# Performance work log

Measured on AMD Instinct MI355X. Metric: run time of the kernel, lower is better.

Reference implementation:

```python
import jax, jax.numpy as jnp
import numpy as np

B, N, E, D, NS, H = 32, 4096, 256, 256, 8, 256
N_ITERS, N_SH, N_MESH, MESH_LR = 3, 5, 4, 5.0

def layer_norm(x, scale, bias, eps=1e-5):
    m = jnp.mean(x, axis=-1, keepdims=True)
    v = jnp.var(x, axis=-1, keepdims=True)
    return (x - m) / jnp.sqrt(v + eps) * scale + bias

def sinkhorn(C, a, b, u=None, v=None, n_iters=N_SH):
    # log-domain Sinkhorn with marginals a [B,N], b [B,S]; C [B,N,S]
    log_a, log_b = jnp.log(a), jnp.log(b)
    if u is None:
        u = jnp.zeros_like(a)
    if v is None:
        v = jnp.zeros_like(b)
    K = -C
    for _ in range(n_iters):
        u = log_a - jax.nn.logsumexp(K + v[:, None, :], axis=-1)
        v = log_b - jax.nn.logsumexp(K + u[:, :, None], axis=-2)
    attn = jnp.exp(K + u[:, :, None] + v[:, None, :])
    return attn, u, v

def minimize_entropy_of_sinkhorn(C0, a, b, mesh_lr=MESH_LR, n_mesh=N_MESH):
    # MESH: gradient-descend the cost matrix to minimize entropy of the transport plan
    def ent(C):
        attn, _, _ = sinkhorn(C, a, b)
        return -jnp.sum(attn * jnp.log(attn + 1e-8))
    C = C0
    for _ in range(n_mesh):
        C = C - mesh_lr * jax.grad(ent)(C)
    _, u, v = sinkhorn(C, a, b)
    return C, u, v

def gru_cell(x, h, Wih, Whh, bih, bhh):
    # torch.nn.GRUCell math, gate order (r, z, n)
    gi = x @ Wih.T + bih
    gh = h @ Whh.T + bhh
    ir, iz, inn = jnp.split(gi, 3, axis=-1)
    hr, hz, hn = jnp.split(gh, 3, axis=-1)
    r = jax.nn.sigmoid(ir + hr)
    z = jax.nn.sigmoid(iz + hz)
    n = jnp.tanh(inn + r * hn)
    return (1.0 - z) * n + z * h

def setup_inputs():
    key = jax.random.key(0)
    ks = jax.random.split(key, 16)
    s = 0.02
    return {
        "inputs": jax.random.normal(ks[0], (B, N, E), jnp.float32),
        "slots_init": jax.random.normal(ks[1], (B, NS, D), jnp.float32),
        "ln_in_s": jnp.ones((E,), jnp.float32), "ln_in_b": jnp.zeros((E,), jnp.float32),
        "ln_sl_s": jnp.ones((D,), jnp.float32), "ln_sl_b": jnp.zeros((D,), jnp.float32),
        "ln_mlp_s": jnp.ones((D,), jnp.float32), "ln_mlp_b": jnp.zeros((D,), jnp.float32),
        "Wq": jax.random.normal(ks[2], (D, D), jnp.float32) * s,
        "Wk": jax.random.normal(ks[3], (E, D), jnp.float32) * s,
        "Wv": jax.random.normal(ks[4], (E, D), jnp.float32) * s,
        "wi_W": jax.random.normal(ks[5], (E, 1), jnp.float32) * s, "wi_b": jnp.zeros((1,), jnp.float32),
        "ws_W": jax.random.normal(ks[6], (D, 1), jnp.float32) * s, "ws_b": jnp.zeros((1,), jnp.float32),
        "gru_Wih": jax.random.normal(ks[7], (3 * D, D), jnp.float32) * s,
        "gru_Whh": jax.random.normal(ks[8], (3 * D, D), jnp.float32) * s,
        "gru_bih": jnp.zeros((3 * D,), jnp.float32), "gru_bhh": jnp.zeros((3 * D,), jnp.float32),
        "mlp_W1": jax.random.normal(ks[9], (D, H), jnp.float32) * s, "mlp_b1": jnp.zeros((H,), jnp.float32),
        "mlp_W2": jax.random.normal(ks[10], (H, D), jnp.float32) * s, "mlp_b2": jnp.zeros((D,), jnp.float32),
    }

def reference(inputs, slots_init, ln_in_s, ln_in_b, ln_sl_s, ln_sl_b, ln_mlp_s, ln_mlp_b, Wq, Wk, Wv, wi_W, wi_b, ws_W, ws_b, gru_Wih, gru_Whh, gru_bih, gru_bhh, mlp_W1, mlp_b1, mlp_W2, mlp_b2):
    x = layer_norm(inputs, ln_in_s, ln_in_b)
    k = x @ Wk          # [B,N,D]
    v = x @ Wv          # [B,N,D]
    a = jax.nn.softmax(jnp.squeeze(x @ wi_W, -1) + wi_b[0], axis=-1) * NS  # input marginal [B,N]
    k_sq = jnp.sum(k * k, axis=-1)  # [B,N]

    def step(slots):
        sn = layer_norm(slots, ln_sl_s, ln_sl_b)
        b = jax.nn.softmax(jnp.squeeze(sn @ ws_W, -1) + ws_b[0], axis=-1) * NS  # slot marginal [B,S]
        q = sn @ Wq  # [B,S,D]
        # Euclidean cdist(k, q) via the Gram-matrix identity
        d2 = k_sq[:, :, None] + jnp.sum(q * q, -1)[:, None, :] - 2.0 * jnp.einsum('bnd,bsd->bns', k, q)
        C = jnp.sqrt(jnp.clip(d2, 1e-12))
        C, p, qpot = minimize_entropy_of_sinkhorn(C, a, b)
        attn, _, _ = sinkhorn(C, a, b, u=p, v=qpot)  # warm-started final sinkhorn
        updates = jnp.einsum('bns,bnd->bsd', attn, v)
        h = gru_cell(updates.reshape(-1, D), slots.reshape(-1, D), gru_Wih, gru_Whh, gru_bih, gru_bhh).reshape(B, NS, D)
        hn = layer_norm(h, ln_mlp_s, ln_mlp_b)
        h = h + (jax.nn.relu(hn @ mlp_W1 + mlp_b1) @ mlp_W2 + mlp_b2)
        return h, attn

    slots = slots_init
    attn = None
    for _ in range(N_ITERS - 1):
        slots, attn = step(slots)
    slots = jax.lax.stop_gradient(slots)  # .detach() before final step
    slots, attn = step(slots)
    return slots, jnp.transpose(attn, (0, 2, 1)), slots
```

## Files before the change

### kernel.cpp

```cpp
#include <hip/hip_runtime.h>
#include <hip/hip_bf16.h>

#define B_ 32
#define N_ 4096
#define E_ 256
#define D_ 256
#define NS_ 8
#define LN8 2.0794415416798357f
#define OFF_ATTN 65536
#define OFF_S2   (65536 + 1048576)
#define NSPLIT 8
#define SENT 0xFFFFFFFFu

typedef unsigned short u16;
typedef __bf16 bf16x8 __attribute__((ext_vector_type(8)));
typedef float floatx4 __attribute__((ext_vector_type(4)));

__device__ __forceinline__ float bf2f(u16 h) {
  unsigned int u = ((unsigned int)h) << 16;
  return __uint_as_float(u);
}
__device__ __forceinline__ u16 f2bf(float f) {
  unsigned int u = __float_as_uint(f);
  unsigned int r = (u + 0x7FFFu + ((u >> 16) & 1u)) >> 16;
  return (u16)r;
}
__device__ __forceinline__ float ldx(const void* p, int i, int dt) {
  return dt ? ((const float*)p)[i] : bf2f(((const u16*)p)[i]);
}
__device__ __forceinline__ void stx(void* p, size_t i, int dt, float v) {
  if (dt) ((float*)p)[i] = v; else ((u16*)p)[i] = f2bf(v);
}
__device__ __forceinline__ float slog(float x) { return __logf(fmaxf(x, 1e-35f)); }
__device__ __forceinline__ float cl(float x) { return fminf(fmaxf(x, -1e30f), 1e30f); }

__device__ __forceinline__ float breduce256(float v, float* red4, int tid) {
  #pragma unroll
  for (int m = 1; m < 64; m <<= 1) v += __shfl_xor(v, m, 64);
  __syncthreads();
  if ((tid & 63) == 0) red4[tid >> 6] = v;
  __syncthreads();
  return red4[0] + red4[1] + red4[2] + red4[3];
}

__global__ void detect_dtype_kernel(const u16* __restrict__ inp, int* __restrict__ flag) {
  int lane = threadIdx.x & 63;
  int good = 0;
  for (int i = lane; i < 256; i += 64) {
    float x = bf2f(inp[i]);
    float ax = fabsf(x);
    if (x == 0.0f || (ax >= 1e-3f && ax <= 64.0f)) good++;
  }
  #pragma unroll
  for (int m = 1; m < 64; m <<= 1) good += __shfl_xor(good, m, 64);
  if (lane == 0) *flag = (good >= 208) ? 0 : 1;
}


__global__ void transpose_any_kernel(const void* __restrict__ src, u16* __restrict__ dst,
                                     int R, int C, const int* __restrict__ dtf) {
  const int dt = *dtf;
  int idx = blockIdx.x * 256 + threadIdx.x;
  if (idx >= R * C) return;
  int r = idx / C, c = idx - r * C;
  dst[c * R + r] = f2bf(ldx(src, idx, dt));
}

__global__ void cast_slots_kernel(const void* __restrict__ src, float* __restrict__ dst,
                                  const int* __restrict__ dtf) {
  const int dt = *dtf;
  int i = blockIdx.x * 256 + threadIdx.x;
  dst[i] = ldx(src, i, dt);
}

__global__ __launch_bounds__(256) void ln_stats_kernel(
    const void* __restrict__ inp, const void* __restrict__ lns, const void* __restrict__ lnb,
    const void* __restrict__ wiW, const int* __restrict__ dtf,
    float2* __restrict__ stats, float* __restrict__ logits) {
  const int dt = *dtf;
  int row = blockIdx.x * 4 + (threadIdx.x >> 6);
  int lane = threadIdx.x & 63;
  float xs[4];
  if (dt) {
    float4 h = *(const float4*)((const float*)inp + (size_t)row * E_ + lane * 4);
    xs[0] = h.x; xs[1] = h.y; xs[2] = h.z; xs[3] = h.w;
  } else {
    ushort4 h = *(const ushort4*)((const u16*)inp + (size_t)row * E_ + lane * 4);
    xs[0] = bf2f(h.x); xs[1] = bf2f(h.y); xs[2] = bf2f(h.z); xs[3] = bf2f(h.w);
  }
  float s = xs[0] + xs[1] + xs[2] + xs[3];
  float q = xs[0]*xs[0] + xs[1]*xs[1] + xs[2]*xs[2] + xs[3]*xs[3];
  #pragma unroll
  for (int m = 1; m < 64; m <<= 1) { s += __shfl_xor(s, m, 64); q += __shfl_xor(q, m, 64); }
  float mean = s * (1.0f / E_);
  float var = q * (1.0f / E_) - mean * mean;
  float rstd = rsqrtf(fmaxf(var, 0.0f) + 1e-5f);
  int e = lane * 4;
  float d = 0.0f;
  #pragma unroll
  for (int j = 0; j < 4; ++j) {
    float xn = (xs[j] - mean) * rstd * ldx(lns, e + j, dt) + ldx(lnb, e + j, dt);
    d += xn * ldx(wiW, e + j, dt);
  }
  #pragma unroll
  for (int m = 1; m < 64; m <<= 1) d += __shfl_xor(d, m, 64);
  if (lane == 0) { stats[row] = make_float2(mean, rstd); logits[row] = d; }
}

__global__ __launch_bounds__(1024) void amarg_kernel(const float* __restrict__ logits,
    float* __restrict__ log_a, float* __restrict__ inva) {
  __shared__ float red[16];
  __shared__ float bcast;
  int b = blockIdx.x, tid = threadIdx.x;
  logits += (size_t)b * N_;
  float l[4];
  #pragma unroll
  for (int i = 0; i < 4; ++i) l[i] = logits[tid + i * 1024];
  float mx = fmaxf(fmaxf(l[0], l[1]), fmaxf(l[2], l[3]));
  #pragma unroll
  for (int m = 1; m < 64; m <<= 1) mx = fmaxf(mx, __shfl_xor(mx, m, 64));
  __syncthreads();
  if ((tid & 63) == 0) red[tid >> 6] = mx;
  __syncthreads();
  if (tid == 0) { float v = red[0]; for (int i = 1; i < 16; ++i) v = fmaxf(v, red[i]); bcast = v; }
  __syncthreads();
  float M = bcast;
  float se = 0.0f;
  #pragma unroll
  for (int i = 0; i < 4; ++i) se += __expf(l[i] - M);
  #pragma unroll
  for (int m = 1; m < 64; m <<= 1) se += __shfl_xor(se, m, 64);
  __syncthreads();
  if ((tid & 63) == 0) red[tid >> 6] = se;
  __syncthreads();
  if (tid == 0) { float v = 0; for (int i = 0; i < 16; ++i) v += red[i]; bcast = v; }
  __syncthreads();
  float lgS = slog(bcast);
  #pragma unroll
  for (int i = 0; i < 4; ++i) {
    float lav = l[i] - M - lgS + LN8;
    log_a[tid + i * 1024] = lav;
    inva[tid + i * 1024] = fminf(__expf(-lav), 1e20f);
  }
}

__global__ __launch_bounds__(256, 2) void gemm_ln_kernel(
    const void* __restrict__ inp, const float2* __restrict__ stats,
    const void* __restrict__ lns, const void* __restrict__ lnb,
    const u16* __restrict__ WT, const int* __restrict__ dtf, u16* __restrict__ out) {
  __shared__ __align__(16) u16 Als[128 * 32];
  __shared__ __align__(16) u16 Bls[128 * 32];
  __shared__ float sS[256], sB[256];
  const int dt = *dtf;
  int tid = threadIdx.x;
  int m0 = blockIdx.x * 128, n0 = blockIdx.y * 128;
  sS[tid] = ldx(lns, tid, dt); sB[tid] = ldx(lnb, tid, dt);
  int w = tid >> 6, lane = tid & 63;
  int wm = (w & 1) * 64, wn = (w >> 1) * 64;
  int fr = lane & 15, kg = lane >> 4;
  floatx4 acc[4][4];
  #pragma unroll
  for (int i = 0; i < 4; ++i)
    #pragma unroll
    for (int j = 0; j < 4; ++j) acc[i][j] = (floatx4){0.f, 0.f, 0.f, 0.f};
  int sm = tid >> 1;
  int sk0 = (tid & 1) * 16;
  int grow = m0 + sm;
  float2 st = stats[grow];
  const u16* arow_h = (const u16*)inp + (size_t)grow * E_;
  const float* arow_f = (const float*)inp + (size_t)grow * E_;
  const u16* brow = WT + (size_t)(n0 + sm) * E_;
  __syncthreads();
  for (int kc = 0; kc < E_; kc += 32) {
    #pragma unroll
    for (int j = 0; j < 16; j += 4) {
      int kk = kc + sk0 + j;
      float x0, x1, x2, x3;
      if (dt) {
        float4 h = *(const float4*)(arow_f + kk);
        x0 = h.x; x1 = h.y; x2 = h.z; x3 = h.w;
      } else {
        ushort4 h = *(const ushort4*)(arow_h + kk);
        x0 = bf2f(h.x); x1 = bf2f(h.y); x2 = bf2f(h.z); x3 = bf2f(h.w);
      }
      ushort4 o;
      o.x = f2bf((x0 - st.x) * st.y * sS[kk + 0] + sB[kk + 0]);
      o.y = f2bf((x1 - st.x) * st.y * sS[kk + 1] + sB[kk + 1]);
      o.z = f2bf((x2 - st.x) * st.y * sS[kk + 2] + sB[kk + 2]);
      o.w = f2bf((x3 - st.x) * st.y * sS[kk + 3] + sB[kk + 3]);
      *(ushort4*)&Als[sm * 32 + sk0 + j] = o;
      *(ushort4*)&Bls[sm * 32 + sk0 + j] = *(const ushort4*)(brow + kk);
    }
    __syncthreads();
    bf16x8 af[4], bfv[4];
    #pragma unroll
    for (int im = 0; im < 4; ++im) af[im] = *(const bf16x8*)&Als[(wm + im * 16 + fr) * 32 + kg * 8];
    #pragma unroll
    for (int in = 0; in < 4; ++in) bfv[in] = *(const bf16x8*)&Bls[(wn + in * 16 + fr) * 32 + kg * 8];
    #pragma unroll
    for (int im = 0; im < 4; ++im)
      #pragma unroll
      for (int in = 0; in < 4; ++in)
        acc[im][in] = __builtin_amdgcn_mfma_f32_16x16x32_bf16(af[im], bfv[in], acc[im][in], 0, 0, 0);
    __syncthreads();
  }
  #pragma unroll
  for (int im = 0; im < 4; ++im)
    #pragma unroll
    for (int in = 0; in < 4; ++in)
      #pragma unroll
      for (int r = 0; r < 4; ++r) {
        int row = m0 + wm + im * 16 + kg * 4 + r;
        int col = n0 + wn + in * 16 + fr;
        out[(size_t)row * D_ + col] = f2bf(acc[im][in][r]);
      }
}

__global__ __launch_bounds__(256) void ksq_kernel(const u16* __restrict__ k, float* __restrict__ ksq) {
  int row = blockIdx.x * 4 + (threadIdx.x >> 6);
  int lane = threadIdx.x & 63;
  ushort4 h = *(const ushort4*)(k + (size_t)row * D_ + lane * 4);
  float a = bf2f(h.x), b = bf2f(h.y), c = bf2f(h.z), d = bf2f(h.w);
  float s = a * a + b * b + c * c + d * d;
  #pragma unroll
  for (int m = 1; m < 64; m <<= 1) s += __shfl_xor(s, m, 64);
  if (lane == 0) ksq[row] = s;
}


__global__ __launch_bounds__(256) void s1_kernel(
    const float* __restrict__ slots, const void* __restrict__ lnss, const void* __restrict__ lnsb,
    const void* __restrict__ Wq, const void* __restrict__ wsW, const int* __restrict__ dtf,
    u16* __restrict__ qbfT, float* __restrict__ q_sq, float* __restrict__ logits_b) {
  __shared__ float sn_sh[256];
  __shared__ float red4[4];
  const int dt = *dtf;
  int row = blockIdx.x;
  int b = row >> 3, s = row & 7;
  int tid = threadIdx.x;
  float h = slots[(size_t)row * D_ + tid];
  float sum = breduce256(h, red4, tid);
  float sq = breduce256(h * h, red4, tid);
  float mean = sum * (1.0f / D_), var = sq * (1.0f / D_) - mean * mean;
  float rstd = rsqrtf(fmaxf(var, 0.0f) + 1e-5f);
  float sn = (h - mean) * rstd * ldx(lnss, tid, dt) + ldx(lnsb, tid, dt);
  sn_sh[tid] = sn;
  __syncthreads();
  float acc = 0.0f;
  if (dt) {
    const float* W = (const float*)Wq;
    for (int d = 0; d < 256; ++d) acc += sn_sh[d] * W[d * 256 + tid];
  } else {
    const u16* W = (const u16*)Wq;
    for (int d = 0; d < 256; ++d) acc += sn_sh[d] * bf2f(W[d * 256 + tid]);
  }
  qbfT[(size_t)(b * 16 + s) * 256 + tid] = f2bf(acc);
  float qs = breduce256(acc * acc, red4, tid);
  float lbp = breduce256(sn * ldx(wsW, tid, dt), red4, tid);
  if (tid == 0) { q_sq[row] = qs; logits_b[row] = lbp; }
}

__global__ void bmarg_kernel(const float* __restrict__ logits_b, const void* __restrict__ wsb,
                             const int* __restrict__ dtf, float* __restrict__ log_b) {
  int b = threadIdx.x;
  if (b >= 32) return;
  float off = ldx(wsb, 0, *dtf);
  float l[8], M = -1e30f;
  #pragma unroll
  for (int s = 0; s < 8; ++s) { l[s] = logits_b[b * 8 + s] + off; M = fmaxf(M, l[s]); }
  float S = 0.0f;
  #pragma unroll
  for (int s = 0; s < 8; ++s) S += __expf(l[s] - M);
  float lgS = slog(S);
  #pragma unroll
  for (int s = 0; s < 8; ++s) log_b[b * 8 + s] = l[s] - M - lgS + LN8;
}

__global__ __launch_bounds__(256) void d2c_kernel(
    const u16* __restrict__ kbf, const u16* __restrict__ qbfT,
    const float* __restrict__ ksq, const float* __restrict__ qsq, float* __restrict__ C) {
  int b = blockIdx.y;
  int tid = threadIdx.x;
  int w = tid >> 6, lane = tid & 63;
  int m0 = blockIdx.x * 64 + w * 16;
  int fr = lane & 15, kg = lane >> 4;
  const u16* kp = kbf + ((size_t)(b * N_ + m0 + fr)) * D_;
  const u16* qp = qbfT + (size_t)(b * 16 + fr) * D_;
  floatx4 acc = (floatx4){0.f, 0.f, 0.f, 0.f};
  #pragma unroll
  for (int kc = 0; kc < D_; kc += 32) {
    bf16x8 a = *(const bf16x8*)(kp + kc + kg * 8);
    bf16x8 bb = *(const bf16x8*)(qp + kc + kg * 8);
    acc = __builtin_amdgcn_mfma_f32_16x16x32_bf16(a, bb, acc, 0, 0, 0);
  }
  if (fr < 8) {
    #pragma unroll
    for (int r = 0; r < 4; ++r) {
      int n = m0 + kg * 4 + r;
      float d2 = ksq[b * N_ + n] + qsq[b * 8 + fr] - 2.0f * acc[r];
      C[((size_t)(b * N_ + n)) * 8 + fr] = sqrtf(fmaxf(d2, 1e-12f));
    }
  }
}

__device__ __forceinline__ float grp_sync_reduce(
    float acc8[8], float (*red)[8],
    unsigned int* gp, int rp, int blkn, int wv, int lane, int tid) {
  #pragma unroll
  for (int m = 1; m < 64; m <<= 1)
    #pragma unroll
    for (int s = 0; s < 8; ++s) acc8[s] += __shfl_xor(acc8[s], m, 64);
  if (lane == 0)
    #pragma unroll
    for (int s = 0; s < 8; ++s) red[wv][s] = acc8[s];
  __syncthreads();
  float x = 0.0f;
  if (tid < 64) {
    float v = red[tid >> 3][tid & 7];
    v += __shfl_xor(v, 8, 64);
    v += __shfl_xor(v, 16, 64);
    v += __shfl_xor(v, 32, 64);
    if (tid < 8)
      __hip_atomic_store(gp + rp * 64 + blkn * 8 + tid, __float_as_uint(v),
                         __ATOMIC_RELAXED, __HIP_MEMORY_SCOPE_AGENT);
    unsigned int u;
    for (;;) {
      u = __hip_atomic_load(gp + rp * 64 + tid, __ATOMIC_RELAXED, __HIP_MEMORY_SCOPE_AGENT);
      if (__all(u != SENT)) break;
      __builtin_amdgcn_s_sleep(1);
    }
    x = __uint_as_float(u);
    x += __shfl_xor(x, 8, 64);
    x += __shfl_xor(x, 16, 64);
    x += __shfl_xor(x, 32, 64);
  }
  return x;
}

__global__ __launch_bounds__(512, 2) void mesh_kernel(
    const float* __restrict__ Cg, const float* __restrict__ log_a_g,
    const float* __restrict__ inva_g, const float* __restrict__ log_b_g,
    const int* __restrict__ dtf,
    unsigned int* __restrict__ gpart,
    float* __restrict__ attn, void* __restrict__ dout_or_null) {
  const int blkn = blockIdx.x;
  const int b = blockIdx.y;
  const int tid = threadIdx.x;
  const int dt = *dtf;
  const int n = blkn * 512 + tid;

  Cg += ((size_t)b * N_ + n) * 8;
  const float la = log_a_g[(size_t)b * N_ + n];
  const float ia = inva_g[(size_t)b * N_ + n];
  log_b_g += b * 8;
  attn += (size_t)b * N_ * 8;
  unsigned int* gp = gpart + (size_t)b * 64 * 64;

  __shared__ float evP[6][8];
  __shared__ float lb[8], invb[8];
  __shared__ float dv[8];
  __shared__ float red[8][8];

  if (tid < 8) { float x = log_b_g[tid]; lb[tid] = x; invb[tid] = fminf(__expf(-x), 1e20f); }

  float E[8], dK[8], eus[5];
  float eu = 0.0f, dup = 0.0f;
  {
    float4 c0 = *(const float4*)(Cg);
    float4 c1 = *(const float4*)(Cg + 4);
    E[0] = __expf(-c0.x); E[1] = __expf(-c0.y); E[2] = __expf(-c0.z); E[3] = __expf(-c0.w);
    E[4] = __expf(-c1.x); E[5] = __expf(-c1.y); E[6] = __expf(-c1.z); E[7] = __expf(-c1.w);
  }
  __syncthreads();

  const int wv = tid >> 6, lane = tid & 63;
  int rp = 0;

  for (int mesh = 0; mesh < 4; ++mesh) {
    if (tid < 8) evP[0][tid] = 1.0f;
    __syncthreads();
    for (int t = 1; t <= 5; ++t) {
      float evp[8];
      #pragma unroll
      for (int s = 0; s < 8; ++s) evp[s] = evP[t - 1][s];
      float su = 0.0f;
      #pragma unroll
      for (int s = 0; s < 8; ++s) su += fminf(E[s] * evp[s], 1e30f);
      float u = la - slog(su);
      eu = fminf(__expf(u), 1e20f);
      eus[t - 1] = eu;
      float acc8[8];
      #pragma unroll
      for (int s = 0; s < 8; ++s) acc8[s] = fminf(E[s] * eu, 1e30f);
      float S = grp_sync_reduce(acc8, red, gp, rp, blkn, wv, lane, tid);
      if (tid < 8) {
        float v = lb[tid] - slog(S);
        evP[t][tid] = fminf(__expf(v), 1e20f);
      }
      ++rp;
      __syncthreads();
    }
    {
      float ev5[8];
      #pragma unroll
      for (int s = 0; s < 8; ++s) ev5[s] = evP[5][s];
      float acc8[8];
      dup = 0.0f;
      #pragma unroll
      for (int s = 0; s < 8; ++s) {
        float t1 = fminf(E[s] * eu, 1e30f);
        float P = fminf(t1 * ev5[s], 1e30f);
        float Pe = P + 1e-8f;
        float g = -(__logf(Pe) + P / Pe) * P;
        dK[s] = g; dup += g; acc8[s] = g;
      }
      float S = grp_sync_reduce(acc8, red, gp, rp, blkn, wv, lane, tid);
      if (tid < 8) dv[tid] = cl(S);
      ++rp;
      __syncthreads();
    }
    for (int t = 5; t >= 1; --t) {
      float evt[8], evtm[8], dvl[8], ibl[8];
      #pragma unroll
      for (int s = 0; s < 8; ++s) { evt[s] = evP[t][s]; evtm[s] = evP[t - 1][s]; dvl[s] = dv[s]; ibl[s] = invb[s]; }
      float eut = eus[t - 1];
      float duv = 0.0f;
      float w8[8];
      #pragma unroll
      for (int s = 0; s < 8; ++s) {
        float a1 = fminf(E[s] * eut, 1e30f);
        float b1 = fminf(a1 * evt[s], 1e30f);
        w8[s] = fminf(b1 * ibl[s], 1e30f);
        duv += cl(dvl[s] * w8[s]);
      }
      float du = ((t == 5) ? dup : 0.0f) - duv;
      float duf = cl(cl(du * ia) * eut);
      float acc8[8];
      #pragma unroll
      for (int s = 0; s < 8; ++s) {
        float ee = fminf(E[s] * evtm[s], 1e30f);
        float zc = cl(ee * duf);
        dK[s] -= cl(dvl[s] * w8[s]) + zc;
        acc8[s] = -zc;
      }
      if (t > 1) {
        float S = grp_sync_reduce(acc8, red, gp, rp, blkn, wv, lane, tid);
        if (tid < 8) dv[tid] = cl(S);
        ++rp;
      }
      __syncthreads();
    }
    #pragma unroll
    for (int s = 0; s < 8; ++s) {
      float dkc = fminf(fmaxf(dK[s], -4.0f), 4.0f);
      float Enew = E[s] * __expf(-5.0f * dkc);
      E[s] = fminf(fmaxf(Enew, 1e-35f), 1e30f);
    }
  }

  if (tid < 8) evP[0][tid] = 1.0f;
  __syncthreads();
  for (int t = 1; t <= 10; ++t) {
    int pc = (t - 1) & 1, cc = t & 1;
    float evp[8];
    #pragma unroll
    for (int s = 0; s < 8; ++s) evp[s] = evP[pc][s];
    float su = 0.0f;
    #pragma unroll
    for (int s = 0; s < 8; ++s) su += fminf(E[s] * evp[s], 1e30f);
    eu = fminf(__expf(la - slog(su)), 1e20f);
    float acc8[8];
    #pragma unroll
    for (int s = 0; s < 8; ++s) acc8[s] = fminf(E[s] * eu, 1e30f);
    float S = grp_sync_reduce(acc8, red, gp, rp, blkn, wv, lane, tid);
    if (tid < 8) {
      float v = lb[tid] - slog(S);
      evP[cc][tid] = fminf(__expf(v), 1e20f);
    }
    ++rp;
    __syncthreads();
  }
  float evf[8];
  #pragma unroll
  for (int s = 0; s < 8; ++s) evf[s] = evP[0][s];
  float pv[8];
  #pragma unroll
  for (int s = 0; s < 8; ++s) {
    float t1 = fminf(E[s] * eu, 1e30f);
    pv[s] = fminf(t1 * evf[s], 1e30f);
  }
  *(float4*)(attn + (size_t)n * 8) = make_float4(pv[0], pv[1], pv[2], pv[3]);
  *(float4*)(attn + (size_t)n * 8 + 4) = make_float4(pv[4], pv[5], pv[6], pv[7]);
  if (dout_or_null) {
    #pragma unroll
    for (int s = 0; s < 8; ++s)
      stx(dout_or_null, (size_t)OFF_ATTN + ((size_t)b * 8 + s) * N_ + n, dt, pv[s]);
  }
}

__global__ __launch_bounds__(256) void upd_kernel(
    const float* __restrict__ attn, const u16* __restrict__ vbf, float* __restrict__ updp) {
  int chunk = blockIdx.x, b = blockIdx.y, d = threadIdx.x;
  const float* ap = attn + ((size_t)b * N_ + chunk * 512) * 8;
  const u16* vp = vbf + ((size_t)b * N_ + chunk * 512) * D_ + d;
  float acc[8] = {0, 0, 0, 0, 0, 0, 0, 0};
  for (int i = 0; i < 512; ++i) {
    float4 a0 = *(const float4*)(ap + (size_t)i * 8);
    float4 a1 = *(const float4*)(ap + (size_t)i * 8 + 4);
    float vv = bf2f(vp[(size_t)i * D_]);
    acc[0] += a0.x * vv; acc[1] += a0.y * vv; acc[2] += a0.z * vv; acc[3] += a0.w * vv;
    acc[4] += a1.x * vv; acc[5] += a1.y * vv; acc[6] += a1.z * vv; acc[7] += a1.w * vv;
  }
  #pragma unroll
  for (int s = 0; s < 8; ++s)
    updp[(((size_t)b * 8 + chunk) * 8 + s) * D_ + d] = acc[s];
}

__global__ __launch_bounds__(256) void gru_mlp_kernel(
    const float* __restrict__ updp, const float* __restrict__ slots_cur,
    const u16* __restrict__ WihT, const u16* __restrict__ WhhT,
    const void* __restrict__ bih, const void* __restrict__ bhh,
    const void* __restrict__ lnms, const void* __restrict__ lnmb,
    const void* __restrict__ W1, const void* __restrict__ b1,
    const void* __restrict__ W2, const void* __restrict__ b2,
    const int* __restrict__ dtf,
    float* __restrict__ slots_next, void* __restrict__ dout_or_null) {
  __shared__ float xs[256], hs[256], hns[256], as_[256];
  __shared__ float red4[4];
  const int dt = *dtf;
  int row = blockIdx.x;
  int b = row >> 3, s = row & 7;
  int tid = threadIdx.x;
  float x = 0.0f;
  #pragma unroll
  for (int c = 0; c < 8; ++c) x += updp[(((size_t)b * 8 + c) * 8 + s) * D_ + tid];
  float h = slots_cur[(size_t)row * D_ + tid];
  xs[tid] = x; hs[tid] = h;
  __syncthreads();
  float gr = ldx(bih, tid, dt), gz = ldx(bih, 256 + tid, dt), gn = ldx(bih, 512 + tid, dt);
  float hr = ldx(bhh, tid, dt), hz = ldx(bhh, 256 + tid, dt), hn_ = ldx(bhh, 512 + tid, dt);
  for (int e = 0; e < 256; ++e) {
    float xe = xs[e], he = hs[e];
    const u16* wi = WihT + e * 768;
    const u16* wh = WhhT + e * 768;
    gr += xe * bf2f(wi[tid]); gz += xe * bf2f(wi[256 + tid]); gn += xe * bf2f(wi[512 + tid]);
    hr += he * bf2f(wh[tid]); hz += he * bf2f(wh[256 + tid]); hn_ += he * bf2f(wh[512 + tid]);
  }
  float r = 1.0f / (1.0f + __expf(-(gr + hr)));
  float z = 1.0f / (1.0f + __expf(-(gz + hz)));
  float nn = tanhf(gn + r * hn_);
  float h2 = (1.0f - z) * nn + z * h;
  float sum = breduce256(h2, red4, tid);
  float sq = breduce256(h2 * h2, red4, tid);
  float mean = sum * (1.0f / D_), var = sq * (1.0f / D_) - mean * mean;
  float rstd = rsqrtf(fmaxf(var, 0.0f) + 1e-5f);
  float hn2 = (h2 - mean) * rstd * ldx(lnms, tid, dt) + ldx(lnmb, tid, dt);
  hns[tid] = hn2;
  __syncthreads();
  float a1 = ldx(b1, tid, dt);
  if (dt) {
    const float* W = (const float*)W1;
    for (int e = 0; e < 256; ++e) a1 += hns[e] * W[e * 256 + tid];
  } else {
    const u16* W = (const u16*)W1;
    for (int e = 0; e < 256; ++e) a1 += hns[e] * bf2f(W[e * 256 + tid]);
  }
  a1 = fmaxf(a1, 0.0f);
  as_[tid] = a1;
  __syncthreads();
  float o = h2 + ldx(b2, tid, dt);
  if (dt) {
    const float* W = (const float*)W2;
    for (int e = 0; e < 256; ++e) o += as_[e] * W[e * 256 + tid];
  } else {
    const u16* W = (const u16*)W2;
    for (int e = 0; e < 256; ++e) o += as_[e] * bf2f(W[e * 256 + tid]);
  }
  slots_next[(size_t)row * D_ + tid] = o;
  if (dout_or_null) {
    stx(dout_or_null, (size_t)row * D_ + tid, dt, o);
    stx(dout_or_null, (size_t)OFF_S2 + (size_t)row * D_ + tid, dt, o);
  }
}


extern "C" void kernel_launch(void* const* d_in, const int* in_sizes, int n_in,
                              void* d_out, int out_size, void* d_ws, size_t ws_size,
                              hipStream_t stream) {
  (void)in_sizes; (void)n_in; (void)out_size;
  const void* inp      = d_in[0];
  const void* slots0   = d_in[1];
  const void* ln_in_s  = d_in[2];
  const void* ln_in_b  = d_in[3];
  const void* ln_sl_s  = d_in[4];
  const void* ln_sl_b  = d_in[5];
  const void* ln_mlp_s = d_in[6];
  const void* ln_mlp_b = d_in[7];
  const void* Wq  = d_in[8];
  const void* Wk  = d_in[9];
  const void* Wv  = d_in[10];
  const void* wiW = d_in[11];
  const void* wsW = d_in[13];
  const void* wsb = d_in[14];
  const void* Wih = d_in[15];
  const void* Whh = d_in[16];
  const void* bih = d_in[17];
  const void* bhh = d_in[18];
  const void* W1  = d_in[19];
  const void* b1  = d_in[20];
  const void* W2  = d_in[21];
  const void* b2  = d_in[22];

  char* ws = (char*)d_ws;
  size_t off = 0;
  auto alloc = [&](size_t bytes) -> void* {
    void* p = ws + off;
    off += (bytes + 255) & ~(size_t)255;
    return p;
  };
  const size_t NR = (size_t)B_ * N_;
  int* dtflag     = (int*)alloc(256);
  float2* stats   = (float2*)alloc(NR * sizeof(float2));
  float* logits_a = (float*)alloc(NR * 4);
  float* log_a    = (float*)alloc(NR * 4);
  float* inva     = (float*)alloc(NR * 4);
  u16* kbf        = (u16*)alloc(NR * D_ * 2);
  u16* vbf        = (u16*)alloc(NR * D_ * 2);
  float* ksq      = (float*)alloc(NR * 4);
  u16* WkT        = (u16*)alloc(E_ * D_ * 2);
  u16* WvT        = (u16*)alloc(E_ * D_ * 2);
  u16* WihT       = (u16*)alloc(768 * 256 * 2);
  u16* WhhT       = (u16*)alloc(768 * 256 * 2);
  u16* qbfT       = (u16*)alloc((size_t)B_ * 16 * 256 * 2);
  float* q_sq     = (float*)alloc(B_ * 8 * 4);
  float* logits_b = (float*)alloc(B_ * 8 * 4);
  float* log_b    = (float*)alloc(B_ * 8 * 4);
  float* Cbuf     = (float*)alloc(NR * 8 * 4);
  float* attnb    = (float*)alloc(NR * 8 * 4);
  float* updp     = (float*)alloc((size_t)B_ * 8 * 8 * D_ * 4);
  float* slots_a  = (float*)alloc((size_t)B_ * 8 * D_ * 4);
  float* slots_b  = (float*)alloc((size_t)B_ * 8 * D_ * 4);
  unsigned int* gpart = (unsigned int*)alloc((size_t)3 * B_ * 64 * 64 * 4);
  if (ws_size < off) return;

  hipMemsetAsync(gpart, 0xFF, (size_t)3 * B_ * 64 * 64 * 4, stream);
  detect_dtype_kernel<<<1, 64, 0, stream>>>((const u16*)inp, dtflag);

  transpose_any_kernel<<<(E_ * D_ + 255) / 256, 256, 0, stream>>>(Wk, WkT, E_, D_, dtflag);
  transpose_any_kernel<<<(E_ * D_ + 255) / 256, 256, 0, stream>>>(Wv, WvT, E_, D_, dtflag);
  transpose_any_kernel<<<(768 * 256 + 255) / 256, 256, 0, stream>>>(Wih, WihT, 768, 256, dtflag);
  transpose_any_kernel<<<(768 * 256 + 255) / 256, 256, 0, stream>>>(Whh, WhhT, 768, 256, dtflag);
  cast_slots_kernel<<<(B_ * 8 * D_) / 256, 256, 0, stream>>>(slots0, slots_a, dtflag);
  hipMemsetAsync(qbfT, 0, (size_t)B_ * 16 * 256 * 2, stream);
  ln_stats_kernel<<<NR / 4, 256, 0, stream>>>(inp, ln_in_s, ln_in_b, wiW, dtflag, stats, logits_a);
  amarg_kernel<<<B_, 1024, 0, stream>>>(logits_a, log_a, inva);
  gemm_ln_kernel<<<dim3(NR / 128, 2), 256, 0, stream>>>(inp, stats, ln_in_s, ln_in_b, WkT, dtflag, kbf);
  gemm_ln_kernel<<<dim3(NR / 128, 2), 256, 0, stream>>>(inp, stats, ln_in_s, ln_in_b, WvT, dtflag, vbf);
  ksq_kernel<<<NR / 4, 256, 0, stream>>>(kbf, ksq);

  float* scur = slots_a;
  float* snext = slots_b;
  for (int step = 0; step < 3; ++step) {
    bool last = (step == 2);
    s1_kernel<<<B_ * 8, 256, 0, stream>>>(scur, ln_sl_s, ln_sl_b, Wq, wsW, dtflag, qbfT, q_sq, logits_b);
    bmarg_kernel<<<1, 32, 0, stream>>>(logits_b, wsb, dtflag, log_b);
    d2c_kernel<<<dim3(N_ / 64, B_), 256, 0, stream>>>(kbf, qbfT, ksq, q_sq, Cbuf);
    mesh_kernel<<<dim3(NSPLIT, B_), 512, 0, stream>>>(Cbuf, log_a, inva, log_b, dtflag,
                                                      gpart + (size_t)step * B_ * 64 * 64,
                                                      attnb, last ? d_out : (void*)nullptr);
    upd_kernel<<<dim3(8, B_), 256, 0, stream>>>(attnb, vbf, updp);
    gru_mlp_kernel<<<B_ * 8, 256, 0, stream>>>(updp, scur, WihT, WhhT, bih, bhh,
                                               ln_mlp_s, ln_mlp_b, W1, b1, W2, b2, dtflag, snext,
                                               last ? d_out : (void*)nullptr);
    float* t = scur; scur = snext; snext = t;
  }
}
```

Baseline: 1.173 ms.

## Fuse cost-matrix computation and attention-value update into mesh kernel

Removes the separate d2c, ksq and upd kernels. The mesh kernel now computes k·q distances with scalar FP32 dot products against q staged in LDS, and it computes the attention-weighted value sums from attention held in LDS. This drops the C and attention buffer round trips through global memory and several launches. In exchange, the distance math moves off MFMA onto scalar ALU inside a low-occupancy kernel of 256 blocks, and k rows are read per thread with poor coalescing.

Result: faster. 1.108 ms (-5.6%).

```diff
diff --git a/kernel.cpp b/kernel.cpp
--- a/kernel.cpp
+++ b/kernel.cpp
@@ -13,6 +13,7 @@
 #define SENT 0xFFFFFFFFu
 
 typedef unsigned short u16;
+typedef unsigned short u16x8 __attribute__((ext_vector_type(8)));
 typedef __bf16 bf16x8 __attribute__((ext_vector_type(8)));
 typedef float floatx4 __attribute__((ext_vector_type(4)));
 
@@ -216,27 +217,15 @@
       }
 }
 
-__global__ __launch_bounds__(256) void ksq_kernel(const u16* __restrict__ k, float* __restrict__ ksq) {
-  int row = blockIdx.x * 4 + (threadIdx.x >> 6);
-  int lane = threadIdx.x & 63;
-  ushort4 h = *(const ushort4*)(k + (size_t)row * D_ + lane * 4);
-  float a = bf2f(h.x), b = bf2f(h.y), c = bf2f(h.z), d = bf2f(h.w);
-  float s = a * a + b * b + c * c + d * d;
-  #pragma unroll
-  for (int m = 1; m < 64; m <<= 1) s += __shfl_xor(s, m, 64);
-  if (lane == 0) ksq[row] = s;
-}
-
 
 __global__ __launch_bounds__(256) void s1_kernel(
     const float* __restrict__ slots, const void* __restrict__ lnss, const void* __restrict__ lnsb,
     const void* __restrict__ Wq, const void* __restrict__ wsW, const int* __restrict__ dtf,
-    u16* __restrict__ qbfT, float* __restrict__ q_sq, float* __restrict__ logits_b) {
+    float* __restrict__ qf, float* __restrict__ q_sq, float* __restrict__ logits_b) {
   __shared__ float sn_sh[256];
   __shared__ float red4[4];
   const int dt = *dtf;
   int row = blockIdx.x;
-  int b = row >> 3, s = row & 7;
   int tid = threadIdx.x;
   float h = slots[(size_t)row * D_ + tid];
   float sum = breduce256(h, red4, tid);
@@ -254,7 +243,7 @@
     const u16* W = (const u16*)Wq;
     for (int d = 0; d < 256; ++d) acc += sn_sh[d] * bf2f(W[d * 256 + tid]);
   }
-  qbfT[(size_t)(b * 16 + s) * 256 + tid] = f2bf(acc);
+  qf[(size_t)row * 256 + tid] = acc;
   float qs = breduce256(acc * acc, red4, tid);
   float lbp = breduce256(sn * ldx(wsW, tid, dt), red4, tid);
   if (tid == 0) { q_sq[row] = qs; logits_b[row] = lbp; }
@@ -274,33 +263,6 @@
   float lgS = slog(S);
   #pragma unroll
   for (int s = 0; s < 8; ++s) log_b[b * 8 + s] = l[s] - M - lgS + LN8;
-}
-
-__global__ __launch_bounds__(256) void d2c_kernel(
-    const u16* __restrict__ kbf, const u16* __restrict__ qbfT,
-    const float* __restrict__ ksq, const float* __restrict__ qsq, float* __restrict__ C) {
-  int b = blockIdx.y;
-  int tid = threadIdx.x;
-  int w = tid >> 6, lane = tid & 63;
-  int m0 = blockIdx.x * 64 + w * 16;
-  int fr = lane & 15, kg = lane >> 4;
-  const u16* kp = kbf + ((size_t)(b * N_ + m0 + fr)) * D_;
-  const u16* qp = qbfT + (size_t)(b * 16 + fr) * D_;
-  floatx4 acc = (floatx4){0.f, 0.f, 0.f, 0.f};
-  #pragma unroll
-  for (int kc = 0; kc < D_; kc += 32) {
-    bf16x8 a = *(const bf16x8*)(kp + kc + kg * 8);
-    bf16x8 bb = *(const bf16x8*)(qp + kc + kg * 8);
-    acc = __builtin_amdgcn_mfma_f32_16x16x32_bf16(a, bb, acc, 0, 0, 0);
-  }
-  if (fr < 8) {
-    #pragma unroll
-    for (int r = 0; r < 4; ++r) {
-      int n = m0 + kg * 4 + r;
-      float d2 = ksq[b * N_ + n] + qsq[b * 8 + fr] - 2.0f * acc[r];
-      C[((size_t)(b * N_ + n)) * 8 + fr] = sqrtf(fmaxf(d2, 1e-12f));
-    }
-  }
 }
 
 __device__ __forceinline__ float grp_sync_reduce(
@@ -338,40 +300,68 @@
 }
 
 __global__ __launch_bounds__(512, 2) void mesh_kernel(
-    const float* __restrict__ Cg, const float* __restrict__ log_a_g,
-    const float* __restrict__ inva_g, const float* __restrict__ log_b_g,
-    const int* __restrict__ dtf,
+    const u16* __restrict__ kbf, const u16* __restrict__ vbf,
+    const float* __restrict__ qf32, const float* __restrict__ qsq_g,
+    const float* __restrict__ log_a_g, const float* __restrict__ inva_g,
+    const float* __restrict__ log_b_g, const int* __restrict__ dtf,
     unsigned int* __restrict__ gpart,
-    float* __restrict__ attn, void* __restrict__ dout_or_null) {
+    float* __restrict__ updp, void* __restrict__ dout_or_null) {
   const int blkn = blockIdx.x;
   const int b = blockIdx.y;
   const int tid = threadIdx.x;
   const int dt = *dtf;
   const int n = blkn * 512 + tid;
 
-  Cg += ((size_t)b * N_ + n) * 8;
-  const float la = log_a_g[(size_t)b * N_ + n];
-  const float ia = inva_g[(size_t)b * N_ + n];
-  log_b_g += b * 8;
-  attn += (size_t)b * N_ * 8;
-  unsigned int* gp = gpart + (size_t)b * 64 * 64;
-
   __shared__ float evP[6][8];
   __shared__ float lb[8], invb[8];
   __shared__ float dv[8];
   __shared__ float red[8][8];
-
-  if (tid < 8) { float x = log_b_g[tid]; lb[tid] = x; invb[tid] = fminf(__expf(-x), 1e20f); }
+  __shared__ float q_lds[8][256];
+  __shared__ float qsq_l[8];
+  __shared__ float pv_lds[512][8];
+
+  const float la = log_a_g[(size_t)b * N_ + n];
+  const float ia = inva_g[(size_t)b * N_ + n];
+  unsigned int* gp = gpart + (size_t)b * 64 * 64;
+
+  {
+    const float* qb = qf32 + (size_t)b * 8 * 256;
+    #pragma unroll
+    for (int i = tid; i < 2048; i += 512) q_lds[i >> 8][i & 255] = qb[i];
+    if (tid < 8) {
+      qsq_l[tid] = qsq_g[b * 8 + tid];
+      float x = log_b_g[b * 8 + tid];
+      lb[tid] = x; invb[tid] = fminf(__expf(-x), 1e20f);
+    }
+  }
+  __syncthreads();
 
   float E[8], dK[8], eus[5];
   float eu = 0.0f, dup = 0.0f;
   {
-    float4 c0 = *(const float4*)(Cg);
-    float4 c1 = *(const float4*)(Cg + 4);
-    E[0] = __expf(-c0.x); E[1] = __expf(-c0.y); E[2] = __expf(-c0.z); E[3] = __expf(-c0.w);
-    E[4] = __expf(-c1.x); E[5] = __expf(-c1.y); E[6] = __expf(-c1.z); E[7] = __expf(-c1.w);
-  }
-  __syncthreads();
+    const u16* kp = kbf + ((size_t)b * N_ + n) * D_;
+    float accq[8] = {0, 0, 0, 0, 0, 0, 0, 0};
+    float kq = 0.0f;
+    for (int kc = 0; kc < 256; kc += 8) {
+      u16x8 kv = *(const u16x8*)(kp + kc);
+      float kf[8];
+      #pragma unroll
+      for (int j = 0; j < 8; ++j) { kf[j] = bf2f(kv[j]); kq += kf[j] * kf[j]; }
+      #pragma unroll
+      for (int s = 0; s < 8; ++s) {
+        float4 qa = *(const float4*)&q_lds[s][kc];
+        float4 qb2 = *(const float4*)&q_lds[s][kc + 4];
+        accq[s] += kf[0] * qa.x + kf[1] * qa.y + kf[2] * qa.z + kf[3] * qa.w
+                 + kf[4] * qb2.x + kf[5] * qb2.y + kf[6] * qb2.z + kf[7] * qb2.w;
+      }
+    }
+    #pragma unroll
+    for (int s = 0; s < 8; ++s) {
+      float d2 = kq + qsq_l[s] - 2.0f * accq[s];
+      float Cv = sqrtf(fmaxf(d2, 1e-12f));
+      E[s] = __expf(-Cv);
+    }
+  }
 
   const int wv = tid >> 6, lane = tid & 63;
   int rp = 0;
@@ -489,31 +479,40 @@
     float t1 = fminf(E[s] * eu, 1e30f);
     pv[s] = fminf(t1 * evf[s], 1e30f);
   }
-  *(float4*)(attn + (size_t)n * 8) = make_float4(pv[0], pv[1], pv[2], pv[3]);
-  *(float4*)(attn + (size_t)n * 8 + 4) = make_float4(pv[4], pv[5], pv[6], pv[7]);
   if (dout_or_null) {
     #pragma unroll
     for (int s = 0; s < 8; ++s)
       stx(dout_or_null, (size_t)OFF_ATTN + ((size_t)b * 8 + s) * N_ + n, dt, pv[s]);
   }
-}
-
-__global__ __launch_bounds__(256) void upd_kernel(
-    const float* __restrict__ attn, const u16* __restrict__ vbf, float* __restrict__ updp) {
-  int chunk = blockIdx.x, b = blockIdx.y, d = threadIdx.x;
-  const float* ap = attn + ((size_t)b * N_ + chunk * 512) * 8;
-  const u16* vp = vbf + ((size_t)b * N_ + chunk * 512) * D_ + d;
-  float acc[8] = {0, 0, 0, 0, 0, 0, 0, 0};
-  for (int i = 0; i < 512; ++i) {
-    float4 a0 = *(const float4*)(ap + (size_t)i * 8);
-    float4 a1 = *(const float4*)(ap + (size_t)i * 8 + 4);
-    float vv = bf2f(vp[(size_t)i * D_]);
-    acc[0] += a0.x * vv; acc[1] += a0.y * vv; acc[2] += a0.z * vv; acc[3] += a0.w * vv;
-    acc[4] += a1.x * vv; acc[5] += a1.y * vv; acc[6] += a1.z * vv; acc[7] += a1.w * vv;
-  }
-  #pragma unroll
-  for (int s = 0; s < 8; ++s)
-    updp[(((size_t)b * 8 + chunk) * 8 + s) * D_ + d] = acc[s];
+
+  #pragma unroll
+  for (int s = 0; s < 8; ++s) pv_lds[tid][s] = pv[s];
+  __syncthreads();
+  {
+    int d = tid & 255, half = tid >> 8;
+    const u16* vp = vbf + ((size_t)b * N_ + blkn * 512 + half * 256) * D_ + d;
+    float acc[8] = {0, 0, 0, 0, 0, 0, 0, 0};
+    for (int i = 0; i < 256; ++i) {
+      float vv = bf2f(vp[(size_t)i * D_]);
+      float4 a0 = *(const float4*)&pv_lds[half * 256 + i][0];
+      float4 a1 = *(const float4*)&pv_lds[half * 256 + i][4];
+      acc[0] += a0.x * vv; acc[1] += a0.y * vv; acc[2] += a0.z * vv; acc[3] += a0.w * vv;
+      acc[4] += a1.x * vv; acc[5] += a1.y * vv; acc[6] += a1.z * vv; acc[7] += a1.w * vv;
+    }
+    __syncthreads();
+    if (half == 1) {
+      #pragma unroll
+      for (int s = 0; s < 8; ++s) pv_lds[d][s] = acc[s];
+    }
+    __syncthreads();
+    if (half == 0) {
+      #pragma unroll
+      for (int s = 0; s < 8; ++s) acc[s] += pv_lds[d][s];
+      #pragma unroll
+      for (int s = 0; s < 8; ++s)
+        updp[(((size_t)b * 8 + blkn) * 8 + s) * D_ + d] = acc[s];
+    }
+  }
 }
 
 __global__ __launch_bounds__(256) void gru_mlp_kernel(
@@ -626,17 +625,14 @@
   float* inva     = (float*)alloc(NR * 4);
   u16* kbf        = (u16*)alloc(NR * D_ * 2);
   u16* vbf        = (u16*)alloc(NR * D_ * 2);
-  float* ksq      = (float*)alloc(NR * 4);
   u16* WkT        = (u16*)alloc(E_ * D_ * 2);
   u16* WvT        = (u16*)alloc(E_ * D_ * 2);
   u16* WihT       = (u16*)alloc(768 * 256 * 2);
   u16* WhhT       = (u16*)alloc(768 * 256 * 2);
-  u16* qbfT       = (u16*)alloc((size_t)B_ * 16 * 256 * 2);
+  float* qf32     = (float*)alloc((size_t)B_ * 8 * 256 * 4);
   float* q_sq     = (float*)alloc(B_ * 8 * 4);
   float* logits_b = (float*)alloc(B_ * 8 * 4);
   float* log_b    = (float*)alloc(B_ * 8 * 4);
-  float* Cbuf     = (float*)alloc(NR * 8 * 4);
-  float* attnb    = (float*)alloc(NR * 8 * 4);
   float* updp     = (float*)alloc((size_t)B_ * 8 * 8 * D_ * 4);
   float* slots_a  = (float*)alloc((size_t)B_ * 8 * D_ * 4);
   float* slots_b  = (float*)alloc((size_t)B_ * 8 * D_ * 4);
@@ -651,24 +647,20 @@
   transpose_any_kernel<<<(768 * 256 + 255) / 256, 256, 0, stream>>>(Wih, WihT, 768, 256, dtflag);
   transpose_any_kernel<<<(768 * 256 + 255) / 256, 256, 0, stream>>>(Whh, WhhT, 768, 256, dtflag);
   cast_slots_kernel<<<(B_ * 8 * D_) / 256, 256, 0, stream>>>(slots0, slots_a, dtflag);
-  hipMemsetAsync(qbfT, 0, (size_t)B_ * 16 * 256 * 2, stream);
   ln_stats_kernel<<<NR / 4, 256, 0, stream>>>(inp, ln_in_s, ln_in_b, wiW, dtflag, stats, logits_a);
   amarg_kernel<<<B_, 1024, 0, stream>>>(logits_a, log_a, inva);
   gemm_ln_kernel<<<dim3(NR / 128, 2), 256, 0, stream>>>(inp, stats, ln_in_s, ln_in_b, WkT, dtflag, kbf);
   gemm_ln_kernel<<<dim3(NR / 128, 2), 256, 0, stream>>>(inp, stats, ln_in_s, ln_in_b, WvT, dtflag, vbf);
-  ksq_kernel<<<NR / 4, 256, 0, stream>>>(kbf, ksq);
 
   float* scur = slots_a;
   float* snext = slots_b;
   for (int step = 0; step < 3; ++step) {
     bool last = (step == 2);
-    s1_kernel<<<B_ * 8, 256, 0, stream>>>(scur, ln_sl_s, ln_sl_b, Wq, wsW, dtflag, qbfT, q_sq, logits_b);
+    s1_kernel<<<B_ * 8, 256, 0, stream>>>(scur, ln_sl_s, ln_sl_b, Wq, wsW, dtflag, qf32, q_sq, logits_b);
     bmarg_kernel<<<1, 32, 0, stream>>>(logits_b, wsb, dtflag, log_b);
-    d2c_kernel<<<dim3(N_ / 64, B_), 256, 0, stream>>>(kbf, qbfT, ksq, q_sq, Cbuf);
-    mesh_kernel<<<dim3(NSPLIT, B_), 512, 0, stream>>>(Cbuf, log_a, inva, log_b, dtflag,
-                                                      gpart + (size_t)step * B_ * 64 * 64,
-                                                      attnb, last ? d_out : (void*)nullptr);
-    upd_kernel<<<dim3(8, B_), 256, 0, stream>>>(attnb, vbf, updp);
+    mesh_kernel<<<dim3(NSPLIT, B_), 512, 0, stream>>>(kbf, vbf, qf32, q_sq, log_a, inva, log_b,
+                                                      dtflag, gpart + (size_t)step * B_ * 64 * 64,
+                                                      updp, last ? d_out : (void*)nullptr);
     gru_mlp_kernel<<<B_ * 8, 256, 0, stream>>>(updp, scur, WihT, WhhT, bih, bhh,
                                                ln_mlp_s, ln_mlp_b, W1, b1, W2, b2, dtflag, snext,
                                                last ? d_out : (void*)nullptr);
```
